# Kernel tuning notes

Measured on AMD Instinct MI355X. Metric: run time of the kernel, lower is better.

Reference implementation:

```python
import jax, jax.numpy as jnp
import numpy as np

KEEP_P = 0.75  # 1 - dropout_p, dropout_p = 0.25

def setup_inputs() -> dict:
    key = jax.random.key(0)
    k1, k2, k3, k4 = jax.random.split(key, 4)
    B, Sq, Skv, D, Dv = 8, 2048, 2048, 128, 128
    x1 = jax.random.normal(k1, (B, Sq, D), dtype=jnp.float32)
    x2 = jax.random.normal(k2, (B, Skv, D), dtype=jnp.float32)
    x3 = jax.random.normal(k3, (B, Skv, Dv), dtype=jnp.float32)
    # torch Dropout(p): mask = bernoulli(keep_p) / keep_p
    keep = jax.random.bernoulli(k4, KEEP_P, (B, Sq, Skv))
    dropout_mask = keep.astype(jnp.float32) / KEEP_P
    return {"x1": x1, "x2": x2, "x3": x3, "dropout_mask": dropout_mask}

def reference(x1, x2, x3, dropout_mask):
    # scores: [B, Sq, Skv] = x1 @ x2^T (no scale: scale_factor is None)
    scores = jnp.einsum("bqd,bkd->bqk", x1, x2)
    probs = jax.nn.softmax(scores, axis=-1)
    probs = probs * dropout_mask  # dropout with fixed mask
    out = jnp.einsum("bqk,bkv->bqv", probs, x3)  # [B, Sq, Dv]
    return out
```

## Files before the change

kernel.cpp:

```cpp
#include <hip/hip_runtime.h>
#include <stdint.h>

#define SQ 2048
#define SKV 2048
#define DD 128
#define NB 8
#define LOG2E 1.44269504088896340736f
#define M0L 57.70780163555852f

typedef float    f4v __attribute__((ext_vector_type(4)));
typedef __bf16   bf8 __attribute__((ext_vector_type(8)));
typedef _Float16 h8  __attribute__((ext_vector_type(8)));

__device__ __forceinline__ void async16(const void* g, void* l) {
    __builtin_amdgcn_global_load_lds(
        (const __attribute__((address_space(1))) void*)g,
        (__attribute__((address_space(3))) void*)l, 16, 0, 0);
}

__global__ void preprocess(const float* __restrict__ x2, _Float16* __restrict__ Kh,
                           const float* __restrict__ x3, __bf16* __restrict__ VTf) {
    __shared__ __bf16 tile[32][33];
    const int bid = blockIdx.x;
    if (bid < 1024) {
        int tid = bid * 256 + threadIdx.x;
        int d8 = tid & 15;
        int kv = (tid >> 4) & (SKV - 1);
        int b  = tid >> 15;
        const float* p = x2 + ((size_t)b * SKV + kv) * DD + d8 * 8;
        f4v a0 = *(const f4v*)p;
        f4v a1 = *(const f4v*)(p + 4);
        h8 h;
#pragma unroll
        for (int c = 0; c < 4; c++) {
            h[c]     = (_Float16)a0[c];
            h[c + 4] = (_Float16)a1[c];
        }
        int s = d8 >> 2, g = d8 & 3, kb32 = kv >> 5, row = kv & 31;
        int h8idx = s * 128 + ((row >> 4) << 6) + g * 16 + (row & 15);
        *(h8*)(Kh + (size_t)(b * 64 + kb32) * 4096 + (size_t)h8idx * 8) = h;
    } else {
        int t = bid - 1024;
        int kb32 = t & 63, dv0 = ((t >> 6) & 3) * 32, b = t >> 8;
        int tx = threadIdx.x & 31, ty = threadIdx.x >> 5;
        const float* src = x3 + ((size_t)b * SKV + kb32 * 32 + ty) * DD + dv0 + tx;
#pragma unroll
        for (int i = 0; i < 32; i += 8)
            tile[ty + i][tx] = (__bf16)src[(size_t)i * DD];
        __syncthreads();
        int pcol = (tx < 16) ? ((tx >> 2) << 3) + (tx & 3)
                             : (((tx - 16) >> 2) << 3) + 4 + (tx & 3);
        __bf16* base = VTf + (size_t)(b * 64 + kb32) * 4096
                     + ((pcol >> 3) << 7) + (pcol & 7);
#pragma unroll
        for (int i = 0; i < 32; i += 8) {
            int dv = dv0 + ty + i;
            base[((dv >> 4) << 9) + ((dv & 15) << 3)] = tile[tx][ty + i];
        }
    }
}

__global__ __launch_bounds__(256, 2) void attn_kernel(
    const float* __restrict__ Qf, const _Float16* __restrict__ Kh,
    const __bf16* __restrict__ Vt, const float* __restrict__ mask,
    float* __restrict__ O_part, float* __restrict__ l_part,
    int nsp, int kv_len) {
    __shared__ __align__(16) char smem[2][16384];
    const int lin = blockIdx.x;
    const int per_xcd = (NB * nsp) >> 3;
    const int xcd = lin & 7;
    const int idx = lin >> 3;
    const int slice = xcd * per_xcd + (idx >> 4);
    const int qblk = idx & 15;
    const int b = slice / nsp, sid = slice % nsp;
    const int tid = threadIdx.x;
    const int w = tid >> 6, lane = tid & 63;
    const int g = lane >> 4, n = lane & 15;
    const int qb = qblk * 128 + w * 32;
    const int kv0 = sid * kv_len;
    const int kb32_0 = kv0 >> 5;
    const int niter = kv_len >> 5;

    const _Float16* Kt0 = Kh + (size_t)(b * 64 + kb32_0) * 4096;
    const __bf16*   Vt0 = Vt + (size_t)(b * 64 + kb32_0) * 4096;
    auto stage = [&](int buf, int it) {
#pragma unroll
        for (int jj = 0; jj < 4; jj++) {
            int j = w * 4 + jj;
            if (j < 8)
                async16(Kt0 + (size_t)it * 4096 + j * 512 + lane * 8,
                        (void*)&smem[buf][j * 1024]);
            else
                async16(Vt0 + (size_t)it * 4096 + (j - 8) * 512 + lane * 8,
                        (void*)&smem[buf][8192 + (j - 8) * 1024]);
        }
    };
    stage(0, 0);

    h8 qf[2][4];
#pragma unroll
    for (int u = 0; u < 2; u++) {
        const float* Qrow = Qf + ((size_t)b * SQ + qb + u * 16 + n) * DD + g * 8;
#pragma unroll
        for (int s = 0; s < 4; s++) {
            f4v v0 = *(const f4v*)(Qrow + s * 32);
            f4v v1 = *(const f4v*)(Qrow + s * 32 + 4);
#pragma unroll
            for (int c = 0; c < 4; c++) {
                qf[u][s][c]     = (_Float16)v0[c];
                qf[u][s][c + 4] = (_Float16)v1[c];
            }
        }
    }

    const float* mrow0 = mask + ((size_t)b * SQ + qb + n) * SKV + kv0;
    const float* mrow1 = mrow0 + (size_t)16 * SKV;
    f4v c00 = *(const f4v*)(mrow0 + g * 4);
    f4v c01 = *(const f4v*)(mrow0 + 16 + g * 4);
    f4v c10 = *(const f4v*)(mrow1 + g * 4);
    f4v c11 = *(const f4v*)(mrow1 + 16 + g * 4);

    const f4v zero = {0.f, 0.f, 0.f, 0.f};
    f4v o0[8], o1[8];
#pragma unroll
    for (int t = 0; t < 8; t++) { o0[t] = zero; o1[t] = zero; }
    float l0 = 0.f, l1 = 0.f;

    for (int it = 0; it < niter; it++) {
        __syncthreads();
        if (it + 1 < niter) stage((it + 1) & 1, it + 1);
        const int itn = (it + 1 < niter) ? it + 1 : it;
        f4v n00 = *(const f4v*)(mrow0 + itn * 32 + g * 4);
        f4v n01 = *(const f4v*)(mrow0 + itn * 32 + 16 + g * 4);
        f4v n10 = *(const f4v*)(mrow1 + itn * 32 + g * 4);
        f4v n11 = *(const f4v*)(mrow1 + itn * 32 + 16 + g * 4);

        const _Float16* Lk = (const _Float16*)smem[it & 1];
        const __bf16*   Lv = (const __bf16*)(smem[it & 1] + 8192);

        f4v s00 = zero, s01 = zero, s10 = zero, s11 = zero;
#pragma unroll
        for (int s = 0; s < 4; s++) {
            h8 a0 = *(const h8*)(Lk + (size_t)(s * 128 + g * 16 + n) * 8);
            h8 a1 = *(const h8*)(Lk + (size_t)(s * 128 + 64 + g * 16 + n) * 8);
            s00 = __builtin_amdgcn_mfma_f32_16x16x32_f16(a0, qf[0][s], s00, 0, 0, 0);
            s01 = __builtin_amdgcn_mfma_f32_16x16x32_f16(a1, qf[0][s], s01, 0, 0, 0);
            s10 = __builtin_amdgcn_mfma_f32_16x16x32_f16(a0, qf[1][s], s10, 0, 0, 0);
            s11 = __builtin_amdgcn_mfma_f32_16x16x32_f16(a1, qf[1][s], s11, 0, 0, 0);
        }

        bf8 pf0, pf1;
#pragma unroll
        for (int r = 0; r < 4; r++) {
            float e00 = exp2f(s00[r] * LOG2E - M0L);
            float e01 = exp2f(s01[r] * LOG2E - M0L);
            float e10 = exp2f(s10[r] * LOG2E - M0L);
            float e11 = exp2f(s11[r] * LOG2E - M0L);
            l0 += e00 + e01;
            l1 += e10 + e11;
            pf0[r]     = (__bf16)(e00 * c00[r]);
            pf0[r + 4] = (__bf16)(e01 * c01[r]);
            pf1[r]     = (__bf16)(e10 * c10[r]);
            pf1[r + 4] = (__bf16)(e11 * c11[r]);
        }

#pragma unroll
        for (int t = 0; t < 8; t++) {
            bf8 vf = *(const bf8*)(Lv + (size_t)(t * 64 + g * 16 + n) * 8);
            o0[t] = __builtin_amdgcn_mfma_f32_16x16x32_bf16(pf0, vf, o0[t], 0, 0, 0);
            o1[t] = __builtin_amdgcn_mfma_f32_16x16x32_bf16(pf1, vf, o1[t], 0, 0, 0);
        }
        c00 = n00; c01 = n01; c10 = n10; c11 = n11;
    }

    l0 += __shfl_xor(l0, 16); l0 += __shfl_xor(l0, 32);
    l1 += __shfl_xor(l1, 16); l1 += __shfl_xor(l1, 32);
    const int qt = qblk * 8 + w * 2;
    const int tile0 = (b * 128 + qt) * nsp + sid;
    const int tile1 = (b * 128 + qt + 1) * nsp + sid;
    float* op0 = O_part + (size_t)tile0 * 2048;
    float* op1 = O_part + (size_t)tile1 * 2048;
#pragma unroll
    for (int t = 0; t < 8; t++)
#pragma unroll
        for (int r = 0; r < 4; r++) {
            op0[(g * 4 + r) * 128 + t * 16 + n] = o0[t][r];
            op1[(g * 4 + r) * 128 + t * 16 + n] = o1[t][r];
        }
    if (g == 0) {
        l_part[(size_t)tile0 * 16 + n] = l0;
        l_part[(size_t)tile1 * 16 + n] = l1;
    }
}

__global__ __launch_bounds__(256) void combine_kernel(
    const float* __restrict__ O_part, const float* __restrict__ l_part,
    float* __restrict__ out, int nsp) {
    const int qt = blockIdx.x;
    const int b  = blockIdx.y;
    const int tbase = (b * 128 + qt) * nsp;
    const int q  = threadIdx.x >> 4;
    const int d8 = threadIdx.x & 15;
    f4v a0 = {0.f, 0.f, 0.f, 0.f}, a1 = {0.f, 0.f, 0.f, 0.f};
    float L = 0.f;
    for (int s = 0; s < nsp; s++) {
        const float* op = O_part + (size_t)(tbase + s) * 2048 + q * 128 + d8 * 8;
        a0 += *(const f4v*)op;
        a1 += *(const f4v*)(op + 4);
        L  += l_part[(size_t)(tbase + s) * 16 + q];
    }
    float scale = 1.0f / L;
    float* o = out + ((size_t)b * SQ + qt * 16 + q) * DD + d8 * 8;
    *(f4v*)o       = a0 * scale;
    *(f4v*)(o + 4) = a1 * scale;
}

extern "C" void kernel_launch(void* const* d_in, const int* in_sizes, int n_in,
                              void* d_out, int out_size, void* d_ws, size_t ws_size,
                              hipStream_t stream) {
    const float* x1   = (const float*)d_in[0];
    const float* x2   = (const float*)d_in[1];
    const float* x3   = (const float*)d_in[2];
    const float* mask = (const float*)d_in[3];
    float* out = (float*)d_out;

    const size_t kelems = (size_t)NB * SKV * DD;
    _Float16* Kh  = (_Float16*)d_ws;
    __bf16*   VTf = (__bf16*)(Kh + kelems);
    float*    O_part = (float*)(VTf + kelems);

    size_t base = 2 * kelems * 2;
    size_t per  = (size_t)NB * 128 * (2048 + 16) * sizeof(float);
    int nsp = 8;
    while (nsp > 1 && base + (size_t)nsp * per > ws_size) nsp >>= 1;
    float* l_part = O_part + (size_t)NB * 128 * nsp * 2048;

    hipLaunchKernelGGL(preprocess, dim3(3072), dim3(256), 0, stream,
                       x2, Kh, x3, VTf);
    hipLaunchKernelGGL(attn_kernel, dim3(16 * NB * nsp), dim3(256), 0, stream,
                       x1, Kh, VTf, mask, O_part, l_part, nsp, SKV / nsp);
    hipLaunchKernelGGL(combine_kernel, dim3(128, NB), dim3(256), 0, stream,
                       O_part, l_part, out, nsp);
}
```

Measured before the change: 251.7 us.

## Pack dropout mask into bitmask in preprocess and read bits in attention

Adds a preprocess stage that reads the fp32 dropout mask with fully coalesced wave-wide loads and uses ballots to pack it into a 1-bit-per-element layout matched to the attention kernel's MFMA fragments. The attention kernel then loads one 32-bit word per row per KV tile instead of four strided float4 mask loads, and rebuilds the mask value as 0 or 1/keep_p. The 128 MB mask still has to be read once, now in a streaming pass that can run at higher bandwidth. In exchange the change adds a 4 MB bitmask write and read, and it assumes mask values are exactly 0 or 1/0.75 as the dropout definition specifies.

```diff
diff --git a/kernel.cpp b/kernel.cpp
--- a/kernel.cpp
+++ b/kernel.cpp
@@ -7,6 +7,7 @@
 #define NB 8
 #define LOG2E 1.44269504088896340736f
 #define M0L 57.70780163555852f
+#define KEEP_INV 1.3333333333333333f
 
 typedef float    f4v __attribute__((ext_vector_type(4)));
 typedef __bf16   bf8 __attribute__((ext_vector_type(8)));
@@ -19,7 +20,8 @@
 }
 
 __global__ void preprocess(const float* __restrict__ x2, _Float16* __restrict__ Kh,
-                           const float* __restrict__ x3, __bf16* __restrict__ VTf) {
+                           const float* __restrict__ x3, __bf16* __restrict__ VTf,
+                           const float* __restrict__ mask, unsigned* __restrict__ bm) {
     __shared__ __bf16 tile[32][33];
     const int bid = blockIdx.x;
     if (bid < 1024) {
@@ -39,7 +41,7 @@
         int s = d8 >> 2, g = d8 & 3, kb32 = kv >> 5, row = kv & 31;
         int h8idx = s * 128 + ((row >> 4) << 6) + g * 16 + (row & 15);
         *(h8*)(Kh + (size_t)(b * 64 + kb32) * 4096 + (size_t)h8idx * 8) = h;
-    } else {
+    } else if (bid < 3072) {
         int t = bid - 1024;
         int kb32 = t & 63, dv0 = ((t >> 6) & 3) * 32, b = t >> 8;
         int tx = threadIdx.x & 31, ty = threadIdx.x >> 5;
@@ -57,12 +59,39 @@
             int dv = dv0 + ty + i;
             base[((dv >> 4) << 9) + ((dv & 15) << 3)] = tile[tx][ty + i];
         }
+    } else {
+        int W = (bid - 3072) * 4 + (threadIdx.x >> 6);
+        int lane = threadIdx.x & 63;
+#pragma unroll 1
+        for (int i = 0; i < 16; i++) {
+            int t  = W * 16 + i;
+            int c8 = t & 7;
+            int row = (t >> 3) & 2047;
+            int b  = t >> 14;
+            f4v v = *(const f4v*)(mask + ((size_t)b * SQ + row) * SKV
+                                  + c8 * 256 + lane * 4);
+            unsigned long long bal[4];
+#pragma unroll
+            for (int c = 0; c < 4; c++)
+                bal[c] = __ballot(v[c] > 0.5f);
+            if (lane == 0) {
+                unsigned* dst = bm + ((size_t)b * 64 + c8 * 8) * 2048 + row;
+#pragma unroll
+                for (int T = 0; T < 8; T++) {
+                    unsigned w = 0;
+#pragma unroll
+                    for (int c = 0; c < 4; c++)
+                        w |= (unsigned)((bal[c] >> (8 * T)) & 0xFFull) << (8 * c);
+                    dst[(size_t)T * 2048] = w;
+                }
+            }
+        }
     }
 }
 
 __global__ __launch_bounds__(256, 2) void attn_kernel(
     const float* __restrict__ Qf, const _Float16* __restrict__ Kh,
-    const __bf16* __restrict__ Vt, const float* __restrict__ mask,
+    const __bf16* __restrict__ Vt, const unsigned* __restrict__ bm,
     float* __restrict__ O_part, float* __restrict__ l_part,
     int nsp, int kv_len) {
     __shared__ __align__(16) char smem[2][16384];
@@ -113,12 +142,8 @@
         }
     }
 
-    const float* mrow0 = mask + ((size_t)b * SQ + qb + n) * SKV + kv0;
-    const float* mrow1 = mrow0 + (size_t)16 * SKV;
-    f4v c00 = *(const f4v*)(mrow0 + g * 4);
-    f4v c01 = *(const f4v*)(mrow0 + 16 + g * 4);
-    f4v c10 = *(const f4v*)(mrow1 + g * 4);
-    f4v c11 = *(const f4v*)(mrow1 + 16 + g * 4);
+    const unsigned* bmb = bm + ((size_t)b * 64 + kb32_0) * 2048 + qb + n;
+    unsigned wc0 = bmb[0], wc1 = bmb[16];
 
     const f4v zero = {0.f, 0.f, 0.f, 0.f};
     f4v o0[8], o1[8];
@@ -130,10 +155,8 @@
         __syncthreads();
         if (it + 1 < niter) stage((it + 1) & 1, it + 1);
         const int itn = (it + 1 < niter) ? it + 1 : it;
-        f4v n00 = *(const f4v*)(mrow0 + itn * 32 + g * 4);
-        f4v n01 = *(const f4v*)(mrow0 + itn * 32 + 16 + g * 4);
-        f4v n10 = *(const f4v*)(mrow1 + itn * 32 + g * 4);
-        f4v n11 = *(const f4v*)(mrow1 + itn * 32 + 16 + g * 4);
+        unsigned wn0 = bmb[(size_t)itn * 2048];
+        unsigned wn1 = bmb[(size_t)itn * 2048 + 16];
 
         const _Float16* Lk = (const _Float16*)smem[it & 1];
         const __bf16*   Lv = (const __bf16*)(smem[it & 1] + 8192);
@@ -149,6 +172,7 @@
             s11 = __builtin_amdgcn_mfma_f32_16x16x32_f16(a1, qf[1][s], s11, 0, 0, 0);
         }
 
+        unsigned a0b = wc0 >> g, a1b = wc1 >> g;
         bf8 pf0, pf1;
 #pragma unroll
         for (int r = 0; r < 4; r++) {
@@ -158,10 +182,14 @@
             float e11 = exp2f(s11[r] * LOG2E - M0L);
             l0 += e00 + e01;
             l1 += e10 + e11;
-            pf0[r]     = (__bf16)(e00 * c00[r]);
-            pf0[r + 4] = (__bf16)(e01 * c01[r]);
-            pf1[r]     = (__bf16)(e10 * c10[r]);
-            pf1[r + 4] = (__bf16)(e11 * c11[r]);
+            float m00 = ((a0b >> (8 * r)) & 1u)     ? KEEP_INV : 0.f;
+            float m01 = ((a0b >> (8 * r + 4)) & 1u) ? KEEP_INV : 0.f;
+            float m10 = ((a1b >> (8 * r)) & 1u)     ? KEEP_INV : 0.f;
+            float m11 = ((a1b >> (8 * r + 4)) & 1u) ? KEEP_INV : 0.f;
+            pf0[r]     = (__bf16)(e00 * m00);
+            pf0[r + 4] = (__bf16)(e01 * m01);
+            pf1[r]     = (__bf16)(e10 * m10);
+            pf1[r + 4] = (__bf16)(e11 * m11);
         }
 
 #pragma unroll
@@ -170,7 +198,7 @@
             o0[t] = __builtin_amdgcn_mfma_f32_16x16x32_bf16(pf0, vf, o0[t], 0, 0, 0);
             o1[t] = __builtin_amdgcn_mfma_f32_16x16x32_bf16(pf1, vf, o1[t], 0, 0, 0);
         }
-        c00 = n00; c01 = n01; c10 = n10; c11 = n11;
+        wc0 = wn0; wc1 = wn1;
     }
 
     l0 += __shfl_xor(l0, 16); l0 += __shfl_xor(l0, 32);
@@ -229,16 +257,18 @@
     __bf16*   VTf = (__bf16*)(Kh + kelems);
     float*    O_part = (float*)(VTf + kelems);
 
-    size_t base = 2 * kelems * 2;
+    size_t bm_sz = (size_t)NB * 64 * 2048 * 4;
+    size_t base = 2 * kelems * 2 + bm_sz;
     size_t per  = (size_t)NB * 128 * (2048 + 16) * sizeof(float);
     int nsp = 8;
     while (nsp > 1 && base + (size_t)nsp * per > ws_size) nsp >>= 1;
-    float* l_part = O_part + (size_t)NB * 128 * nsp * 2048;
-
-    hipLaunchKernelGGL(preprocess, dim3(3072), dim3(256), 0, stream,
-                       x2, Kh, x3, VTf);
+    float*    l_part = O_part + (size_t)NB * 128 * nsp * 2048;
+    unsigned* bm     = (unsigned*)(l_part + (size_t)NB * 128 * nsp * 16);
+
+    hipLaunchKernelGGL(preprocess, dim3(5120), dim3(256), 0, stream,
+                       x2, Kh, x3, VTf, mask, bm);
     hipLaunchKernelGGL(attn_kernel, dim3(16 * NB * nsp), dim3(256), 0, stream,
-                       x1, Kh, VTf, mask, O_part, l_part, nsp, SKV / nsp);
+                       x1, Kh, VTf, bm, O_part, l_part, nsp, SKV / nsp);
     hipLaunchKernelGGL(combine_kernel, dim3(128, NB), dim3(256), 0, stream,
                        O_part, l_part, out, nsp);
 }
```

New measurement: 270.0 us. 7.3% more time.
